# Kernel optimization log

Hardware: AMD Instinct MI355X
Metric: run time of the kernel (lower is better)

Reference implementation:

```python
import jax, jax.numpy as jnp
import numpy as np

S = 14        # grid size
B = 2         # boxes per cell
NC = 20       # classes
N = 4096      # batch
L_COORD = 5.0
L_NOOBJ = 0.5


def _xywh2xyxy(b):
    # b[..., :2] are cell-center coords (scaled by 1/S), b[..., 2:4] are w,h
    xy = b[..., :2] / S
    wh = b[..., 2:4]
    return jnp.concatenate([xy - 0.5 * wh, xy + 0.5 * wh], axis=-1)


def _iou(b1, b2):
    # elementwise (broadcasting) IoU over last dim [x1,y1,x2,y2]
    lt = jnp.maximum(b1[..., :2], b2[..., :2])
    rb = jnp.minimum(b1[..., 2:4], b2[..., 2:4])
    wh = jnp.clip(rb - lt, 0.0)
    inter = wh[..., 0] * wh[..., 1]
    a1 = (b1[..., 2] - b1[..., 0]) * (b1[..., 3] - b1[..., 1])
    a2 = (b2[..., 2] - b2[..., 0]) * (b2[..., 3] - b2[..., 1])
    return inter / (a1 + a2 - inter)


def setup_inputs() -> dict:
    key = jax.random.key(0)
    k1, k2, k3, k4 = jax.random.split(key, 4)
    pred_tensor = jax.random.uniform(k1, (N, S, S, B * 5 + NC), dtype=jnp.float32)
    target_boxes = jax.random.uniform(k2, (N, S, S, 4), dtype=jnp.float32)
    target_cls = jax.random.uniform(k3, (N, S, S, NC), dtype=jnp.float32)
    has_object_map = jax.random.bernoulli(k4, 0.15, (N, S, S))
    return dict(pred_tensor=pred_tensor, target_boxes=target_boxes,
                target_cls=target_cls, has_object_map=has_object_map)


def reference(pred_tensor, target_boxes, target_cls, has_object_map):
    n = pred_tensor.shape[0]
    pb = pred_tensor[..., :B * 5].reshape(n, S, S, B, 5)   # (N,S,S,B,5)
    pcls = pred_tensor[..., B * 5:]                        # (N,S,S,20)
    m = has_object_map                                     # (N,S,S) bool
    mf = m.astype(pred_tensor.dtype)

    # class loss: masked sum of squares over object cells
    cls_loss = jnp.sum(jnp.where(m[..., None], (pcls - target_cls) ** 2, 0.0))

    # no-object loss: confidence^2 summed over non-object cells, both boxes
    noobj_loss = jnp.sum(jnp.where(~m[..., None], pb[..., 4] ** 2, 0.0))

    # best-iou box selection (iou is treated as ground truth: no gradient)
    iou = _iou(_xywh2xyxy(pb[..., :4]),
               _xywh2xyxy(target_boxes)[..., None, :])    # (N,S,S,B)
    iou = jax.lax.stop_gradient(iou)
    best = jnp.argmax(iou, axis=-1)                        # (N,S,S)
    best_iou = jnp.max(iou, axis=-1)                       # (N,S,S)
    resp = jnp.take_along_axis(pb, best[..., None, None], axis=3)[..., 0, :]  # (N,S,S,5)

    reg_loss = (jnp.sum(mf[..., None] * (resp[..., :2] - target_boxes[..., :2]) ** 2)
                + jnp.sum(mf[..., None] * (jnp.sqrt(resp[..., 2:4])
                                           - jnp.sqrt(target_boxes[..., 2:4])) ** 2))

    # containing-object confidence loss vs best iou (target detached)
    contain_loss = jnp.sum(mf * (resp[..., 4] - best_iou) ** 2)

    total = (L_COORD * reg_loss + L_NOOBJ * noobj_loss + contain_loss + cls_loss) / n
    return jnp.stack([total, reg_loss, contain_loss, noobj_loss, cls_loss])
```

## Files before the change

### kernel.cpp

```cpp
#include <hip/hip_runtime.h>


#define GS 14
#define NCLS 20
#define BLOCK 256
#define CPB 512
#define NSLOTS 64
#define SLOT_STRIDE 16
#define WAVE_F 1920
#define SLAB_F (4 * WAVE_F)


__device__ __forceinline__ void gload_lds16(const float* g, float* l) {
    __builtin_amdgcn_global_load_lds(
        (const __attribute__((address_space(1))) void*)g,
        (__attribute__((address_space(3))) void*)l, 16, 0, 0);
}
__device__ __forceinline__ void gload_lds4(const float* g, float* l) {
    __builtin_amdgcn_global_load_lds(
        (const __attribute__((address_space(1))) void*)g,
        (__attribute__((address_space(3))) void*)l, 4, 0, 0);
}

__device__ __forceinline__ void stage_wave(const float* gsrc, float* ldst, int lane) {
    #pragma unroll
    for (int i = 0; i < 7; ++i)
        gload_lds16(gsrc + i * 256 + lane * 4, ldst + i * 256);
    #pragma unroll
    for (int k = 0; k < 2; ++k)
        gload_lds4(gsrc + 1792 + k * 64 + lane, ldst + 1792 + k * 64);
}

__device__ __forceinline__ void cell_compute(const float (&v)[30],
                                             const float4 tb4,
                                             const float* __restrict__ tcls,
                                             int cell, bool m,
                                             float& reg, float& cont,
                                             float& noobj, float& cls) {
    const float invS = 1.0f / (float)GS;
    if (m) {
        const float tx = tb4.x, ty = tb4.y, tw = tb4.z, th = tb4.w;

        const float tcx = tx * invS, tcy = ty * invS;
        const float t_x1 = tcx - 0.5f * tw, t_y1 = tcy - 0.5f * th;
        const float t_x2 = tcx + 0.5f * tw, t_y2 = tcy + 0.5f * th;
        const float ta = (t_x2 - t_x1) * (t_y2 - t_y1);

        const float b0x = v[0], b0y = v[1], b0w = v[2], b0h = v[3], b0c = v[4];
        const float b1x = v[5], b1y = v[6], b1w = v[7], b1h = v[8], b1c = v[9];

        float iou0, iou1;
        {
            const float cx = b0x * invS, cy = b0y * invS;
            const float x1 = cx - 0.5f * b0w, y1 = cy - 0.5f * b0h;
            const float x2 = cx + 0.5f * b0w, y2 = cy + 0.5f * b0h;
            const float iw = fmaxf(fminf(x2, t_x2) - fmaxf(x1, t_x1), 0.0f);
            const float ih = fmaxf(fminf(y2, t_y2) - fmaxf(y1, t_y1), 0.0f);
            const float inter = iw * ih;
            const float pa = (x2 - x1) * (y2 - y1);
            iou0 = inter / (pa + ta - inter);
        }
        {
            const float cx = b1x * invS, cy = b1y * invS;
            const float x1 = cx - 0.5f * b1w, y1 = cy - 0.5f * b1h;
            const float x2 = cx + 0.5f * b1w, y2 = cy + 0.5f * b1h;
            const float iw = fmaxf(fminf(x2, t_x2) - fmaxf(x1, t_x1), 0.0f);
            const float ih = fmaxf(fminf(y2, t_y2) - fmaxf(y1, t_y1), 0.0f);
            const float inter = iw * ih;
            const float pa = (x2 - x1) * (y2 - y1);
            iou1 = inter / (pa + ta - inter);
        }

        const bool sel1 = iou1 > iou0;
        const float biou = fmaxf(iou0, iou1);
        const float rx = sel1 ? b1x : b0x;
        const float ry = sel1 ? b1y : b0y;
        const float rw = sel1 ? b1w : b0w;
        const float rh = sel1 ? b1h : b0h;
        const float rc = sel1 ? b1c : b0c;

        const float d0 = rx - tx, d1 = ry - ty;
        const float d2 = sqrtf(rw) - sqrtf(tw);
        const float d3 = sqrtf(rh) - sqrtf(th);
        reg += d0 * d0 + d1 * d1 + d2 * d2 + d3 * d3;

        const float dc = rc - biou;
        cont += dc * dc;

        const float4* tc4 = reinterpret_cast<const float4*>(tcls + (size_t)cell * NCLS);
        float csum = 0.0f;
        #pragma unroll
        for (int j = 0; j < 5; ++j) {
            const float4 t4 = tc4[j];
            float d;
            d = v[10 + j * 4 + 0] - t4.x; csum += d * d;
            d = v[10 + j * 4 + 1] - t4.y; csum += d * d;
            d = v[10 + j * 4 + 2] - t4.z; csum += d * d;
            d = v[10 + j * 4 + 3] - t4.w; csum += d * d;
        }
        cls += csum;
    } else {
        const float c0 = v[4], c1 = v[9];
        noobj += c0 * c0 + c1 * c1;
    }
}

__device__ __forceinline__ void ds_read_row(const float* lrow, float (&v)[30]) {
    #pragma unroll
    for (int j = 0; j < 7; ++j)
        *reinterpret_cast<float4*>(&v[j * 4]) =
            *reinterpret_cast<const float4*>(lrow + j * 4);
    *reinterpret_cast<float2*>(&v[28]) =
        *reinterpret_cast<const float2*>(lrow + 28);
}

__launch_bounds__(BLOCK)
__global__ void yolo_loss_kernel(const float* __restrict__ pred,
                                 const float* __restrict__ tbox,
                                 const float* __restrict__ tcls,
                                 const void* __restrict__ mask,
                                 float* __restrict__ ws,
                                 int ncells) {
    __shared__ float slab[SLAB_F];
    const int tid = threadIdx.x;
    const int wv = tid >> 6;
    const int lane = tid & 63;

    int my_bits = 0;
    if (ncells >= 4096) {
        const uint4 w4 = reinterpret_cast<const uint4*>(mask)[tid];
        const unsigned a = w4.x | w4.y | w4.z | w4.w;
        my_bits  = ((a & 0xFEFEFEFEu) != 0) ? 2 : 0;
        my_bits |= ((a & 0xFFFFFF00u) != 0) ? 1 : 0;
    } else if (tid == 0) {
        const unsigned char* mb = (const unsigned char*)mask;
        for (int i = 0; i < ncells; ++i) {
            if (mb[i] > 1) my_bits |= 2;
            if ((i & 3) != 0 && mb[i] != 0) my_bits |= 1;
        }
    }
    const int bits = __syncthreads_or(my_bits);
    const int fmt = (bits & 2) ? 2 : ((bits & 1) ? 1 : 0);

    const int base = blockIdx.x * CPB;

    float reg = 0.0f, cont = 0.0f, noobj = 0.0f, cls = 0.0f;

    if (base + CPB <= ncells) {
        const int cellA = base + wv * 64 + lane;
        const int cellB = cellA + 256;

        const float* gsrcA = pred + (size_t)(base + wv * 64) * 30;
        const float* gsrcB = gsrcA + 256 * 30;
        float* ldst = slab + wv * WAVE_F;
        const float* lrow = ldst + lane * 30;

        stage_wave(gsrcA, ldst, lane);

        bool mA, mB;
        if (fmt == 2) {
            mA = ((const float*)mask)[cellA] != 0.0f;
            mB = ((const float*)mask)[cellB] != 0.0f;
        } else if (fmt == 1) {
            mA = ((const unsigned char*)mask)[cellA] != 0;
            mB = ((const unsigned char*)mask)[cellB] != 0;
        } else {
            mA = ((const int*)mask)[cellA] != 0;
            mB = ((const int*)mask)[cellB] != 0;
        }
        const float4 tbA = reinterpret_cast<const float4*>(tbox)[cellA];
        const float4 tbB = reinterpret_cast<const float4*>(tbox)[cellB];

        asm volatile("s_waitcnt vmcnt(0)" ::: "memory");
        __builtin_amdgcn_sched_barrier(0);

        float vA[30];
        ds_read_row(lrow, vA);

        asm volatile("s_waitcnt lgkmcnt(0)" ::: "memory");
        __builtin_amdgcn_sched_barrier(0);

        stage_wave(gsrcB, ldst, lane);

        cell_compute(vA, tbA, tcls, cellA, mA, reg, cont, noobj, cls);

        asm volatile("s_waitcnt vmcnt(0)" ::: "memory");
        __builtin_amdgcn_sched_barrier(0);

        float vB[30];
        ds_read_row(lrow, vB);

        cell_compute(vB, tbB, tcls, cellB, mB, reg, cont, noobj, cls);
    } else {
        for (int cell = base + tid; cell < ncells; cell += BLOCK) {
            bool m;
            if (fmt == 2)      m = ((const float*)mask)[cell] != 0.0f;
            else if (fmt == 1) m = ((const unsigned char*)mask)[cell] != 0;
            else               m = ((const int*)mask)[cell] != 0;
            float v[30];
            #pragma unroll
            for (int f = 0; f < 30; ++f) v[f] = pred[(size_t)cell * 30 + f];
            float4 tb;
            tb.x = tbox[(size_t)cell * 4 + 0];
            tb.y = tbox[(size_t)cell * 4 + 1];
            tb.z = tbox[(size_t)cell * 4 + 2];
            tb.w = tbox[(size_t)cell * 4 + 3];
            cell_compute(v, tb, tcls, cell, m, reg, cont, noobj, cls);
        }
    }

    #pragma unroll
    for (int off = 32; off > 0; off >>= 1) {
        reg   += __shfl_down(reg, off);
        cont  += __shfl_down(cont, off);
        noobj += __shfl_down(noobj, off);
        cls   += __shfl_down(cls, off);
    }

    __shared__ float sred[4][4];
    if (lane == 0) {
        sred[wv][0] = reg; sred[wv][1] = cont;
        sred[wv][2] = noobj; sred[wv][3] = cls;
    }
    __syncthreads();
    if (tid == 0) {
        float r = 0, c = 0, no = 0, cl = 0;
        #pragma unroll
        for (int w = 0; w < 4; ++w) {
            r += sred[w][0]; c += sred[w][1]; no += sred[w][2]; cl += sred[w][3];
        }
        float* slot = ws + (size_t)(blockIdx.x & (NSLOTS - 1)) * SLOT_STRIDE;
        atomicAdd(&slot[0], r);
        atomicAdd(&slot[1], c);
        atomicAdd(&slot[2], no);
        atomicAdd(&slot[3], cl);
    }
}

__global__ void yolo_finalize_kernel(const float* __restrict__ ws,
                                     float* __restrict__ out, float inv_n) {
    const int t = threadIdx.x;
    float reg   = ws[t * SLOT_STRIDE + 0];
    float cont  = ws[t * SLOT_STRIDE + 1];
    float noobj = ws[t * SLOT_STRIDE + 2];
    float cls   = ws[t * SLOT_STRIDE + 3];
    #pragma unroll
    for (int off = 32; off > 0; off >>= 1) {
        reg   += __shfl_down(reg, off);
        cont  += __shfl_down(cont, off);
        noobj += __shfl_down(noobj, off);
        cls   += __shfl_down(cls, off);
    }
    if (t == 0) {
        const float total = (5.0f * reg + 0.5f * noobj + cont + cls) * inv_n;
        out[0] = total;
        out[1] = reg;
        out[2] = cont;
        out[3] = noobj;
        out[4] = cls;
    }
}

extern "C" void kernel_launch(void* const* d_in, const int* in_sizes, int n_in,
                              void* d_out, int out_size, void* d_ws, size_t ws_size,
                              hipStream_t stream) {
    const float* pred = (const float*)d_in[0];
    const float* tbox = (const float*)d_in[1];
    const float* tcls = (const float*)d_in[2];
    const void*  mask = d_in[3];
    float* ws  = (float*)d_ws;
    float* out = (float*)d_out;

    const int ncells = in_sizes[3];
    const int n_img  = ncells / (GS * GS);
    const float inv_n = 1.0f / (float)n_img;

    hipMemsetAsync(ws, 0, NSLOTS * SLOT_STRIDE * sizeof(float), stream);

    const int grid = (ncells + CPB - 1) / CPB;
    yolo_loss_kernel<<<grid, BLOCK, 0, stream>>>(pred, tbox, tcls, mask, ws, ncells);

    yolo_finalize_kernel<<<1, 64, 0, stream>>>(ws, out, inv_n);
}
```

Before: 33.33 us.

## Double-buffer LDS staging across four rounds per wave with hoisted class loads

```diff
diff --git a/kernel.cpp b/kernel.cpp
--- a/kernel.cpp
+++ b/kernel.cpp
@@ -3,12 +3,18 @@
 
 #define GS 14
 #define NCLS 20
-#define BLOCK 256
-#define CPB 512
+#define BLOCK 128
+#define WAVES 2
+#define ROUNDS 4
+#define WCELLS 64
+#define CPW (ROUNDS * WCELLS)
+#define CPB (WAVES * CPW)
 #define NSLOTS 64
 #define SLOT_STRIDE 16
 #define WAVE_F 1920
-#define SLAB_F (4 * WAVE_F)
+#define SLAB_F (WAVES * 2 * WAVE_F)
+
+#define SB() __builtin_amdgcn_sched_barrier(0)
 
 
 __device__ __forceinline__ void gload_lds16(const float* g, float* l) {
@@ -31,10 +37,31 @@
         gload_lds4(gsrc + 1792 + k * 64 + lane, ldst + 1792 + k * 64);
 }
 
+__device__ __forceinline__ void ds_read_row(const float* lrow, float (&v)[30]) {
+    #pragma unroll
+    for (int j = 0; j < 7; ++j)
+        *reinterpret_cast<float4*>(&v[j * 4]) =
+            *reinterpret_cast<const float4*>(lrow + j * 4);
+    *reinterpret_cast<float2*>(&v[28]) =
+        *reinterpret_cast<const float2*>(lrow + 28);
+}
+
+__device__ __forceinline__ void load_tc(const float* __restrict__ tcls, int cell, bool m,
+                                        float4& t0, float4& t1, float4& t2,
+                                        float4& t3, float4& t4) {
+    t0 = t1 = t2 = t3 = t4 = make_float4(0.f, 0.f, 0.f, 0.f);
+    if (m) {
+        const float4* tp = reinterpret_cast<const float4*>(tcls) + (size_t)cell * 5;
+        t0 = tp[0]; t1 = tp[1]; t2 = tp[2]; t3 = tp[3]; t4 = tp[4];
+    }
+}
+
 __device__ __forceinline__ void cell_compute(const float (&v)[30],
                                              const float4 tb4,
-                                             const float* __restrict__ tcls,
-                                             int cell, bool m,
+                                             const float4 t0, const float4 t1,
+                                             const float4 t2, const float4 t3,
+                                             const float4 t4,
+                                             bool m,
                                              float& reg, float& cont,
                                              float& noobj, float& cls) {
     const float invS = 1.0f / (float)GS;
@@ -87,31 +114,23 @@
         const float dc = rc - biou;
         cont += dc * dc;
 
-        const float4* tc4 = reinterpret_cast<const float4*>(tcls + (size_t)cell * NCLS);
         float csum = 0.0f;
-        #pragma unroll
-        for (int j = 0; j < 5; ++j) {
-            const float4 t4 = tc4[j];
-            float d;
-            d = v[10 + j * 4 + 0] - t4.x; csum += d * d;
-            d = v[10 + j * 4 + 1] - t4.y; csum += d * d;
-            d = v[10 + j * 4 + 2] - t4.z; csum += d * d;
-            d = v[10 + j * 4 + 3] - t4.w; csum += d * d;
-        }
+        float d;
+        d = v[10] - t0.x; csum += d * d;  d = v[11] - t0.y; csum += d * d;
+        d = v[12] - t0.z; csum += d * d;  d = v[13] - t0.w; csum += d * d;
+        d = v[14] - t1.x; csum += d * d;  d = v[15] - t1.y; csum += d * d;
+        d = v[16] - t1.z; csum += d * d;  d = v[17] - t1.w; csum += d * d;
+        d = v[18] - t2.x; csum += d * d;  d = v[19] - t2.y; csum += d * d;
+        d = v[20] - t2.z; csum += d * d;  d = v[21] - t2.w; csum += d * d;
+        d = v[22] - t3.x; csum += d * d;  d = v[23] - t3.y; csum += d * d;
+        d = v[24] - t3.z; csum += d * d;  d = v[25] - t3.w; csum += d * d;
+        d = v[26] - t4.x; csum += d * d;  d = v[27] - t4.y; csum += d * d;
+        d = v[28] - t4.z; csum += d * d;  d = v[29] - t4.w; csum += d * d;
         cls += csum;
     } else {
         const float c0 = v[4], c1 = v[9];
         noobj += c0 * c0 + c1 * c1;
     }
-}
-
-__device__ __forceinline__ void ds_read_row(const float* lrow, float (&v)[30]) {
-    #pragma unroll
-    for (int j = 0; j < 7; ++j)
-        *reinterpret_cast<float4*>(&v[j * 4]) =
-            *reinterpret_cast<const float4*>(lrow + j * 4);
-    *reinterpret_cast<float2*>(&v[28]) =
-        *reinterpret_cast<const float2*>(lrow + 28);
 }
 
 __launch_bounds__(BLOCK)
@@ -127,7 +146,7 @@
     const int lane = tid & 63;
 
     int my_bits = 0;
-    if (ncells >= 4096) {
+    if (ncells >= 2048) {
         const uint4 w4 = reinterpret_cast<const uint4*>(mask)[tid];
         const unsigned a = w4.x | w4.y | w4.z | w4.w;
         my_bits  = ((a & 0xFEFEFEFEu) != 0) ? 2 : 0;
@@ -147,50 +166,72 @@
     float reg = 0.0f, cont = 0.0f, noobj = 0.0f, cls = 0.0f;
 
     if (base + CPB <= ncells) {
-        const int cellA = base + wv * 64 + lane;
-        const int cellB = cellA + 256;
-
-        const float* gsrcA = pred + (size_t)(base + wv * 64) * 30;
-        const float* gsrcB = gsrcA + 256 * 30;
-        float* ldst = slab + wv * WAVE_F;
-        const float* lrow = ldst + lane * 30;
-
-        stage_wave(gsrcA, ldst, lane);
-
-        bool mA, mB;
+        const int wbase = base + wv * CPW;
+        const int ca = wbase + lane;
+        const int cb = ca + 64, cc = ca + 128, cd = ca + 192;
+
+        const float* gsrc = pred + (size_t)wbase * 30;
+        float* R0 = slab + (wv * 2 + 0) * WAVE_F;
+        float* R1 = slab + (wv * 2 + 1) * WAVE_F;
+        const float* rowA = R0 + lane * 30;
+        const float* rowB = R1 + lane * 30;
+
+        stage_wave(gsrc, R0, lane);
+        SB();
+
+        bool mA, mB, mC, mD;
         if (fmt == 2) {
-            mA = ((const float*)mask)[cellA] != 0.0f;
-            mB = ((const float*)mask)[cellB] != 0.0f;
+            const float* mp = (const float*)mask;
+            mA = mp[ca] != 0.0f; mB = mp[cb] != 0.0f;
+            mC = mp[cc] != 0.0f; mD = mp[cd] != 0.0f;
         } else if (fmt == 1) {
-            mA = ((const unsigned char*)mask)[cellA] != 0;
-            mB = ((const unsigned char*)mask)[cellB] != 0;
+            const unsigned char* mp = (const unsigned char*)mask;
+            mA = mp[ca] != 0; mB = mp[cb] != 0;
+            mC = mp[cc] != 0; mD = mp[cd] != 0;
         } else {
-            mA = ((const int*)mask)[cellA] != 0;
-            mB = ((const int*)mask)[cellB] != 0;
-        }
-        const float4 tbA = reinterpret_cast<const float4*>(tbox)[cellA];
-        const float4 tbB = reinterpret_cast<const float4*>(tbox)[cellB];
-
-        asm volatile("s_waitcnt vmcnt(0)" ::: "memory");
-        __builtin_amdgcn_sched_barrier(0);
-
-        float vA[30];
-        ds_read_row(lrow, vA);
-
-        asm volatile("s_waitcnt lgkmcnt(0)" ::: "memory");
-        __builtin_amdgcn_sched_barrier(0);
-
-        stage_wave(gsrcB, ldst, lane);
-
-        cell_compute(vA, tbA, tcls, cellA, mA, reg, cont, noobj, cls);
-
-        asm volatile("s_waitcnt vmcnt(0)" ::: "memory");
-        __builtin_amdgcn_sched_barrier(0);
-
-        float vB[30];
-        ds_read_row(lrow, vB);
-
-        cell_compute(vB, tbB, tcls, cellB, mB, reg, cont, noobj, cls);
+            const int* mp = (const int*)mask;
+            mA = mp[ca] != 0; mB = mp[cb] != 0;
+            mC = mp[cc] != 0; mD = mp[cd] != 0;
+        }
+        const float4* tbp = reinterpret_cast<const float4*>(tbox);
+        const float4 tbA = tbp[ca], tbB = tbp[cb], tbC = tbp[cc], tbD = tbp[cd];
+        SB();
+
+        stage_wave(gsrc + WAVE_F, R1, lane);
+        SB();
+
+        {
+            asm volatile("s_waitcnt vmcnt(9)" ::: "memory"); SB();
+            float v[30]; ds_read_row(rowA, v);
+            asm volatile("s_waitcnt lgkmcnt(0)" ::: "memory"); SB();
+            float4 t0, t1, t2, t3, t4;
+            load_tc(tcls, ca, mA, t0, t1, t2, t3, t4); SB();
+            stage_wave(gsrc + 2 * WAVE_F, R0, lane); SB();
+            cell_compute(v, tbA, t0, t1, t2, t3, t4, mA, reg, cont, noobj, cls);
+        }
+        {
+            asm volatile("s_waitcnt vmcnt(9)" ::: "memory"); SB();
+            float v[30]; ds_read_row(rowB, v);
+            asm volatile("s_waitcnt lgkmcnt(0)" ::: "memory"); SB();
+            float4 t0, t1, t2, t3, t4;
+            load_tc(tcls, cb, mB, t0, t1, t2, t3, t4); SB();
+            stage_wave(gsrc + 3 * WAVE_F, R1, lane); SB();
+            cell_compute(v, tbB, t0, t1, t2, t3, t4, mB, reg, cont, noobj, cls);
+        }
+        {
+            asm volatile("s_waitcnt vmcnt(9)" ::: "memory"); SB();
+            float v[30]; ds_read_row(rowA, v);
+            float4 t0, t1, t2, t3, t4;
+            load_tc(tcls, cc, mC, t0, t1, t2, t3, t4); SB();
+            cell_compute(v, tbC, t0, t1, t2, t3, t4, mC, reg, cont, noobj, cls);
+        }
+        {
+            asm volatile("s_waitcnt vmcnt(0)" ::: "memory"); SB();
+            float v[30]; ds_read_row(rowB, v);
+            float4 t0, t1, t2, t3, t4;
+            load_tc(tcls, cd, mD, t0, t1, t2, t3, t4);
+            cell_compute(v, tbD, t0, t1, t2, t3, t4, mD, reg, cont, noobj, cls);
+        }
     } else {
         for (int cell = base + tid; cell < ncells; cell += BLOCK) {
             bool m;
@@ -205,7 +246,9 @@
             tb.y = tbox[(size_t)cell * 4 + 1];
             tb.z = tbox[(size_t)cell * 4 + 2];
             tb.w = tbox[(size_t)cell * 4 + 3];
-            cell_compute(v, tb, tcls, cell, m, reg, cont, noobj, cls);
+            float4 t0, t1, t2, t3, t4;
+            load_tc(tcls, cell, m, t0, t1, t2, t3, t4);
+            cell_compute(v, tb, t0, t1, t2, t3, t4, m, reg, cont, noobj, cls);
         }
     }
 
@@ -217,7 +260,7 @@
         cls   += __shfl_down(cls, off);
     }
 
-    __shared__ float sred[4][4];
+    __shared__ float sred[WAVES][4];
     if (lane == 0) {
         sred[wv][0] = reg; sred[wv][1] = cont;
         sred[wv][2] = noobj; sred[wv][3] = cls;
@@ -226,7 +269,7 @@
     if (tid == 0) {
         float r = 0, c = 0, no = 0, cl = 0;
         #pragma unroll
-        for (int w = 0; w < 4; ++w) {
+        for (int w = 0; w < WAVES; ++w) {
             r += sred[w][0]; c += sred[w][1]; no += sred[w][2]; cl += sred[w][3];
         }
         float* slot = ws + (size_t)(blockIdx.x & (NSLOTS - 1)) * SLOT_STRIDE;
```

New measurement: 40.79 us. 1.22x slower.
